# Kernel tuning notes

Hardware: AMD Instinct MI355X
Metric: run time of the kernel (lower is better)

Reference implementation:

```python
import jax, jax.numpy as jnp
import numpy as np

N = 100000      # nodes
E = 600000      # directed edges (reciprocal pairs)
D_NODE = 128    # node feature dim (== hidden, required by torch.where broadcast)
D_BOND = 16     # bond feature dim
HID = 128       # hidden size
DEPTH = 3       # message passing depth


def setup_inputs() -> dict:
    key = jax.random.key(0)
    ks = jax.random.split(key, 8)
    x = jax.random.normal(ks[0], (N, D_NODE), jnp.float32)
    # build edges as reciprocal pairs: edge 2i = (u,v), edge 2i+1 = (v,u)
    half = E // 2
    u = jax.random.randint(ks[1], (half,), 0, N)
    v = jax.random.randint(ks[2], (half,), 0, N)
    src = jnp.stack([u, v], axis=1).reshape(-1)
    dst = jnp.stack([v, u], axis=1).reshape(-1)
    edge_index = jnp.stack([src, dst])          # [2, E]
    rev_edge_index = jnp.arange(E) ^ 1           # reverse edge of 2i is 2i+1
    edge_attr = jax.random.normal(ks[3], (E, D_BOND), jnp.float32)
    # learned params (Linear: y = x @ W + b)
    s_i = 1.0 / np.sqrt(D_NODE + D_BOND)
    s_h = 1.0 / np.sqrt(HID)
    s_o = 1.0 / np.sqrt(D_NODE + HID)
    W_i = jax.random.normal(ks[4], (D_NODE + D_BOND, HID), jnp.float32) * s_i
    b_i = jnp.zeros((HID,), jnp.float32)
    W_h = jax.random.normal(ks[5], (HID, HID), jnp.float32) * s_h
    b_h = jnp.zeros((HID,), jnp.float32)
    W_o = jax.random.normal(ks[6], (D_NODE + HID, HID), jnp.float32) * s_o
    b_o = jnp.zeros((HID,), jnp.float32)
    return dict(x=x, edge_attr=edge_attr, W_i=W_i, b_i=b_i, W_h=W_h, b_h=b_h,
                W_o=W_o, b_o=b_o, edge_index=edge_index,
                rev_edge_index=rev_edge_index)


def reference(x, edge_attr, W_i, b_i, W_h, b_h, W_o, b_o,
              edge_index, rev_edge_index):
    src, dst = edge_index[0], edge_index[1]
    # H_0 = relu(W_i([x[src]; edge_attr]))
    H0 = jax.nn.relu(jnp.concatenate([x[src], edge_attr], axis=1) @ W_i + b_i)
    H = H0
    for _ in range(DEPTH - 1):
        # message: scatter-sum over dst, gather by src, subtract reverse edge
        agg = jax.ops.segment_sum(H, dst, num_segments=N)   # [N, HID]
        M = agg[src] - H[rev_edge_index]                    # [E, HID]
        # update: relu(H0 + W_h(M))   (dropout is identity in eval)
        H = jax.nn.relu(H0 + M @ W_h + b_h)
    # final node aggregation
    Mn = jax.ops.segment_sum(H, dst, num_segments=N)        # [N, HID]
    Mn = jnp.where(jnp.sum(Mn, axis=1, keepdims=True) == 0, x, Mn)
    out = jax.nn.relu(jnp.concatenate([x, Mn], axis=1) @ W_o + b_o)  # [N, HID]
    return out
```

## Files before the change

kernel.cpp:

```cpp
#include <hip/hip_runtime.h>
#include <hip/hip_bf16.h>

#define N_NODES 100000
#define N_EDGES 600000
#define HID 128
#define D_BOND 16
#define NB_CHUNKS 98

typedef __attribute__((ext_vector_type(8))) short bf16x8;
typedef __attribute__((ext_vector_type(4))) float f32x4;

__device__ __forceinline__ float bf2f(unsigned int u) {
    return __uint_as_float((u & 0xffffu) << 16);
}
__device__ __forceinline__ unsigned short f2bf(float f) {
    unsigned int x = __float_as_uint(f);
    x += 0x7fffu + ((x >> 16) & 1u);
    return (unsigned short)(x >> 16);
}
__device__ __forceinline__ unsigned int pk2(float a, float b) {
    return (unsigned int)f2bf(a) | ((unsigned int)f2bf(b) << 16);
}

__device__ __forceinline__ void st16(unsigned char* tile, int row, int u, uint4 v) {
    *reinterpret_cast<uint4*>(tile + ((row * 512 + u * 16) ^ ((row & 7) << 4))) = v;
}
__device__ __forceinline__ bf16x8 ld_a(const unsigned char* tile, int row, int kbyte) {
    return *reinterpret_cast<const bf16x8*>(tile + ((row * 512 + kbyte) ^ ((row & 7) << 4)));
}

template<int NK>
__device__ __forceinline__ void gemm_frag(const unsigned char* tile, const unsigned short* Wp,
                                          int wr, int cb, int l, f32x4 (&acc)[4]) {
    const int arow = 16 * wr + (l & 15);
    const int abyte0 = (l >> 4) * 16;
#pragma unroll
    for (int kk = 0; kk < NK; ++kk) {
        const bf16x8 a = ld_a(tile, arow, kk * 64 + abyte0);
#pragma unroll
        for (int c = 0; c < 4; ++c) {
            const bf16x8 b = *reinterpret_cast<const bf16x8*>(&Wp[(((kk * 8) + cb + c) * 64 + l) * 8]);
            acc[c] = __builtin_amdgcn_mfma_f32_16x16x32_bf16(a, b, acc[c], 0, 0, 0);
        }
    }
}

__global__ __launch_bounds__(256) void k_hist(const int* __restrict__ dst,
                                              int* __restrict__ cnt) {
    int e = blockIdx.x * 256 + threadIdx.x;
    if (e < N_EDGES) atomicAdd(&cnt[dst[e]], 1);
}

__global__ __launch_bounds__(256) void k_blocksum(const int* __restrict__ cnt,
                                                  int* __restrict__ bsum) {
    __shared__ int red[256];
    const int b = blockIdx.x, t = threadIdx.x;
    const int base = b * 1024 + t * 4;
    int s = 0;
#pragma unroll
    for (int i = 0; i < 4; ++i) { int n = base + i; if (n < N_NODES) s += cnt[n]; }
    red[t] = s; __syncthreads();
    for (int o = 128; o > 0; o >>= 1) { if (t < o) red[t] += red[t + o]; __syncthreads(); }
    if (t == 0) bsum[b] = red[0];
}

__global__ __launch_bounds__(128) void k_scan_bsum(const int* __restrict__ bsum,
                                                   int* __restrict__ boff,
                                                   int* __restrict__ rowptr) {
    __shared__ int s[128];
    const int t = threadIdx.x;
    const int v = (t < NB_CHUNKS) ? bsum[t] : 0;
    s[t] = v; __syncthreads();
    for (int o = 1; o < 128; o <<= 1) {
        int add = 0; if (t >= o) add = s[t - o];
        __syncthreads();
        s[t] += add; __syncthreads();
    }
    if (t < NB_CHUNKS) boff[t] = s[t] - v;
    if (t == 0) rowptr[N_NODES] = N_EDGES;
}

__global__ __launch_bounds__(256) void k_scan_chunk(const int* __restrict__ cnt,
                                                    const int* __restrict__ boff,
                                                    int* __restrict__ rowptr,
                                                    int* __restrict__ wpos) {
    __shared__ int s[256];
    const int b = blockIdx.x, t = threadIdx.x;
    const int base = b * 1024 + t * 4;
    int v[4]; int ts = 0;
#pragma unroll
    for (int i = 0; i < 4; ++i) { int n = base + i; v[i] = (n < N_NODES) ? cnt[n] : 0; ts += v[i]; }
    s[t] = ts; __syncthreads();
    for (int o = 1; o < 256; o <<= 1) {
        int add = 0; if (t >= o) add = s[t - o];
        __syncthreads();
        s[t] += add; __syncthreads();
    }
    int run = s[t] - ts + boff[b];
#pragma unroll
    for (int i = 0; i < 4; ++i) {
        int n = base + i;
        if (n < N_NODES) { rowptr[n] = run; wpos[n] = run; }
        run += v[i];
    }
}

__global__ __launch_bounds__(256) void k_fill(const int* __restrict__ dst,
                                              int* __restrict__ wpos,
                                              int* __restrict__ eidx) {
    int e = blockIdx.x * 256 + threadIdx.x;
    if (e < N_EDGES) { int p = atomicAdd(&wpos[dst[e]], 1); eidx[p] = e; }
}

__global__ __launch_bounds__(256) void k_pack(const float* __restrict__ Wi,
                                              const float* __restrict__ Wh,
                                              const float* __restrict__ Wo,
                                              unsigned short* __restrict__ Pi,
                                              unsigned short* __restrict__ Ph,
                                              unsigned short* __restrict__ Po) {
    const int tid = blockIdx.x * 256 + threadIdx.x;
    const float* W; unsigned short* P; int Krows, base;
    if (tid < 2560)      { W = Wi; P = Pi; Krows = 144; base = tid; }
    else if (tid < 4608) { W = Wh; P = Ph; Krows = 128; base = tid - 2560; }
    else                 { W = Wo; P = Po; Krows = 256; base = tid - 4608; }
    const int l = base & 63, fc = base >> 6;
    const int c = fc & 7, kk = fc >> 3;
    const int col = c * 16 + (l & 15);
    const int k0 = kk * 32 + (l >> 4) * 8;
    float v[8];
#pragma unroll
    for (int j = 0; j < 8; ++j) {
        const int k = k0 + j;
        v[j] = (k < Krows) ? W[(size_t)k * HID + col] : 0.f;
    }
    uint4 o;
    o.x = pk2(v[0], v[1]); o.y = pk2(v[2], v[3]);
    o.z = pk2(v[4], v[5]); o.w = pk2(v[6], v[7]);
    *reinterpret_cast<uint4*>(&P[(size_t)base * 8]) = o;
}

__device__ __forceinline__ void stage_xe(unsigned char* tile, const float* __restrict__ x,
                                         const float* __restrict__ ea, const int* s_src,
                                         int e0, int t) {
    for (int f = t; f < 512; f += 256) {
        const int e = f >> 4, u = f & 15;
        const float* xp = &x[(size_t)s_src[e] * HID + u * 8];
        const float4 v0 = *reinterpret_cast<const float4*>(xp);
        const float4 v1 = *reinterpret_cast<const float4*>(xp + 4);
        uint4 o;
        o.x = pk2(v0.x, v0.y); o.y = pk2(v0.z, v0.w);
        o.z = pk2(v1.x, v1.y); o.w = pk2(v1.z, v1.w);
        st16(tile, e, u, o);
    }
    if (t < 64) {
        const int e = t >> 1, u = t & 1;
        const float* ep = &ea[(size_t)(e0 + e) * D_BOND + u * 8];
        const float4 v0 = *reinterpret_cast<const float4*>(ep);
        const float4 v1 = *reinterpret_cast<const float4*>(ep + 4);
        uint4 o;
        o.x = pk2(v0.x, v0.y); o.y = pk2(v0.z, v0.w);
        o.z = pk2(v1.x, v1.y); o.w = pk2(v1.z, v1.w);
        st16(tile, e, 16 + u, o);
    } else if (t < 128) {
        const int i = t - 64, e = i >> 1, u = i & 1;
        st16(tile, e, 18 + u, make_uint4(0, 0, 0, 0));
    }
}

__global__ __launch_bounds__(256) void k_h0(const float* __restrict__ x,
                                            const float* __restrict__ ea,
                                            const unsigned short* __restrict__ Pi,
                                            const float* __restrict__ bi,
                                            const int* __restrict__ src,
                                            unsigned short* __restrict__ H) {
    __shared__ __align__(16) unsigned char tile[32 * 512];
    __shared__ int s_src[32];
    const int e0 = blockIdx.x * 32;
    const int t = threadIdx.x;
    if (t < 32) s_src[t] = src[e0 + t];
    __syncthreads();
    stage_xe(tile, x, ea, s_src, e0, t);
    __syncthreads();
    const int w = t >> 6, l = t & 63;
    const int wr = w & 1, cb = (w >> 1) * 4;
    f32x4 acc[4] = {{0.f,0.f,0.f,0.f},{0.f,0.f,0.f,0.f},{0.f,0.f,0.f,0.f},{0.f,0.f,0.f,0.f}};
    gemm_frag<5>(tile, Pi, wr, cb, l, acc);
    const int frow = 16 * wr + 4 * (l >> 4);
#pragma unroll
    for (int c = 0; c < 4; ++c) {
        const int col = ((cb + c) << 4) | (l & 15);
        const float bias = bi[col];
#pragma unroll
        for (int r = 0; r < 4; ++r) {
            H[(size_t)(e0 + frow + r) * HID + col] = f2bf(fmaxf(acc[c][r] + bias, 0.f));
        }
    }
}

__global__ __launch_bounds__(256) void k_agg(const unsigned short* __restrict__ H,
                                             const int* __restrict__ rowptr,
                                             const int* __restrict__ eidx,
                                             void* __restrict__ aggv) {
    const int wid = (blockIdx.x * 256 + threadIdx.x) >> 6;
    const int lane = threadIdx.x & 63;
    if (wid >= N_NODES) return;
    const int beg = rowptr[wid], end = rowptr[wid + 1];
    float a0 = 0.f, a1 = 0.f;
    for (int j = beg; j < end; ++j) {
        const int e = eidx[j];
        const unsigned int p = *reinterpret_cast<const unsigned int*>(&H[(size_t)e * HID + lane * 2]);
        a0 += bf2f(p);
        a1 += bf2f(p >> 16);
    }
    *reinterpret_cast<unsigned int*>((char*)aggv + (size_t)wid * 512 + lane * 4) = pk2(a0, a1);
}

template<int RECOMP>
__global__ __launch_bounds__(256) void k_msg(const float* __restrict__ x,
                                             const float* __restrict__ ea,
                                             const void* __restrict__ aggv,
                                             const unsigned short* __restrict__ Pi,
                                             const float* __restrict__ bi,
                                             const unsigned short* __restrict__ Ph,
                                             const float* __restrict__ bh,
                                             const int* __restrict__ src,
                                             const int* __restrict__ rev,
                                             unsigned short* H) {
    __shared__ __align__(16) unsigned char tile[32 * 512];
    __shared__ int s_src[32], s_rev[32];
    const int e0 = blockIdx.x * 32;
    const int t = threadIdx.x;
    if (t < 32) { s_src[t] = src[e0 + t]; s_rev[t] = rev[e0 + t]; }
    __syncthreads();
    const int w = t >> 6, l = t & 63;
    const int wr = w & 1, cb = (w >> 1) * 4;
    float h0r[4][4];

    if (RECOMP) {
        stage_xe(tile, x, ea, s_src, e0, t);
        __syncthreads();
        f32x4 acc[4] = {{0.f,0.f,0.f,0.f},{0.f,0.f,0.f,0.f},{0.f,0.f,0.f,0.f},{0.f,0.f,0.f,0.f}};
        gemm_frag<5>(tile, Pi, wr, cb, l, acc);
#pragma unroll
        for (int c = 0; c < 4; ++c) {
            const float bias = bi[((cb + c) << 4) | (l & 15)];
#pragma unroll
            for (int r = 0; r < 4; ++r) h0r[c][r] = fmaxf(acc[c][r] + bias, 0.f);
        }
        __syncthreads();
    }

    for (int f = t; f < 512; f += 256) {
        const int e = f >> 4, u = f & 15;
        const unsigned short* ap =
            reinterpret_cast<const unsigned short*>((const char*)aggv + (size_t)s_src[e] * 512) + u * 8;
        const uint4 av = *reinterpret_cast<const uint4*>(ap);
        const uint4 hv = *reinterpret_cast<const uint4*>(&H[(size_t)s_rev[e] * HID + u * 8]);
        uint4 o;
        o.x = pk2(bf2f(av.x) - bf2f(hv.x), bf2f(av.x >> 16) - bf2f(hv.x >> 16));
        o.y = pk2(bf2f(av.y) - bf2f(hv.y), bf2f(av.y >> 16) - bf2f(hv.y >> 16));
        o.z = pk2(bf2f(av.z) - bf2f(hv.z), bf2f(av.z >> 16) - bf2f(hv.z >> 16));
        o.w = pk2(bf2f(av.w) - bf2f(hv.w), bf2f(av.w >> 16) - bf2f(hv.w >> 16));
        st16(tile, e, u, o);
    }
    __syncthreads();
    f32x4 acc[4] = {{0.f,0.f,0.f,0.f},{0.f,0.f,0.f,0.f},{0.f,0.f,0.f,0.f},{0.f,0.f,0.f,0.f}};
    gemm_frag<4>(tile, Ph, wr, cb, l, acc);
    const int frow = 16 * wr + 4 * (l >> 4);
#pragma unroll
    for (int c = 0; c < 4; ++c) {
        const int col = ((cb + c) << 4) | (l & 15);
        const float bias = bh[col];
#pragma unroll
        for (int r = 0; r < 4; ++r) {
            const size_t idx = (size_t)(e0 + frow + r) * HID + col;
            const float h0v = RECOMP ? h0r[c][r] : bf2f((unsigned int)H[idx]);
            H[idx] = f2bf(fmaxf(h0v + acc[c][r] + bias, 0.f));
        }
    }
}

__global__ __launch_bounds__(256) void k_out(const float* __restrict__ x,
                                             const void* aggv,
                                             const int* __restrict__ cnt,
                                             const unsigned short* __restrict__ Po,
                                             const float* __restrict__ bo,
                                             float* out) {
    __shared__ __align__(16) unsigned char tile[32 * 512];
    __shared__ int s_cnt[32];
    const int n0 = blockIdx.x * 32;
    const int t = threadIdx.x;
    if (t < 32) s_cnt[t] = cnt[n0 + t];
    __syncthreads();
    for (int f = t; f < 1024; f += 256) {
        const int e = f >> 5, u = f & 31;
        uint4 o;
        if (u >= 16 && s_cnt[e] > 0) {
            o = *reinterpret_cast<const uint4*>((const char*)aggv + (size_t)(n0 + e) * 512 + (u - 16) * 16);
        } else {
            const int k8 = (u & 15) * 8;
            const float* xp = &x[(size_t)(n0 + e) * HID + k8];
            const float4 v0 = *reinterpret_cast<const float4*>(xp);
            const float4 v1 = *reinterpret_cast<const float4*>(xp + 4);
            o.x = pk2(v0.x, v0.y); o.y = pk2(v0.z, v0.w);
            o.z = pk2(v1.x, v1.y); o.w = pk2(v1.z, v1.w);
        }
        st16(tile, e, u, o);
    }
    __syncthreads();
    const int w = t >> 6, l = t & 63;
    const int wr = w & 1, cb = (w >> 1) * 4;
    f32x4 acc[4] = {{0.f,0.f,0.f,0.f},{0.f,0.f,0.f,0.f},{0.f,0.f,0.f,0.f},{0.f,0.f,0.f,0.f}};
    gemm_frag<8>(tile, Po, wr, cb, l, acc);
    const int frow = 16 * wr + 4 * (l >> 4);
#pragma unroll
    for (int c = 0; c < 4; ++c) {
        const int col = ((cb + c) << 4) | (l & 15);
        const float bias = bo[col];
#pragma unroll
        for (int r = 0; r < 4; ++r) {
            out[(size_t)(n0 + frow + r) * HID + col] = fmaxf(acc[c][r] + bias, 0.f);
        }
    }
}

extern "C" void kernel_launch(void* const* d_in, const int* in_sizes, int n_in,
                              void* d_out, int out_size, void* d_ws, size_t ws_size,
                              hipStream_t stream) {
    const float* x  = (const float*)d_in[0];
    const float* ea = (const float*)d_in[1];
    const float* Wi = (const float*)d_in[2];
    const float* bi = (const float*)d_in[3];
    const float* Wh = (const float*)d_in[4];
    const float* bh = (const float*)d_in[5];
    const float* Wo = (const float*)d_in[6];
    const float* bo = (const float*)d_in[7];
    const int* ei   = (const int*)d_in[8];
    const int* rev  = (const int*)d_in[9];
    const int* src  = ei;
    const int* dst  = ei + N_EDGES;

    char* ws = (char*)d_ws;
    size_t off = 0;
    auto alloc = [&](size_t bytes) -> void* {
        void* p = ws + off;
        off += (bytes + 255) & ~(size_t)255;
        return p;
    };
    unsigned short* H  = (unsigned short*)alloc((size_t)N_EDGES * HID * 2);
    int* cnt     = (int*)alloc((size_t)N_NODES * 4);
    int* rowptr  = (int*)alloc((size_t)(N_NODES + 1) * 4);
    int* wpos    = (int*)alloc((size_t)N_NODES * 4);
    int* bsum    = (int*)alloc(512);
    int* boff    = (int*)alloc(512);
    int* eidx    = (int*)alloc((size_t)N_EDGES * 4);
    unsigned short* Pi = (unsigned short*)alloc(2560 * 8 * 2);
    unsigned short* Ph = (unsigned short*)alloc(2048 * 8 * 2);
    unsigned short* Po = (unsigned short*)alloc(4096 * 8 * 2);
    void* agg = d_out;

    const int EB = (N_EDGES + 255) / 256;

    hipMemsetAsync(cnt, 0, (size_t)N_NODES * 4, stream);
    k_hist<<<EB, 256, 0, stream>>>(dst, cnt);
    k_blocksum<<<NB_CHUNKS, 256, 0, stream>>>(cnt, bsum);
    k_scan_bsum<<<1, 128, 0, stream>>>(bsum, boff, rowptr);
    k_scan_chunk<<<NB_CHUNKS, 256, 0, stream>>>(cnt, boff, rowptr, wpos);
    k_fill<<<EB, 256, 0, stream>>>(dst, wpos, eidx);

    k_pack<<<34, 256, 0, stream>>>(Wi, Wh, Wo, Pi, Ph, Po);

    k_h0<<<N_EDGES / 32, 256, 0, stream>>>(x, ea, Pi, bi, src, H);

    k_agg<<<N_NODES / 4, 256, 0, stream>>>(H, rowptr, eidx, agg);
    k_msg<0><<<N_EDGES / 32, 256, 0, stream>>>(x, ea, agg, Pi, bi, Ph, bh, src, rev, H);

    k_agg<<<N_NODES / 4, 256, 0, stream>>>(H, rowptr, eidx, agg);
    k_msg<1><<<N_EDGES / 32, 256, 0, stream>>>(x, ea, agg, Pi, bi, Ph, bh, src, rev, H);

    k_agg<<<N_NODES / 4, 256, 0, stream>>>(H, rowptr, eidx, agg);
    k_out<<<N_NODES / 32, 256, 0, stream>>>(x, agg, cnt, Po, bo, (float*)d_out);
}
```

Measured before the change: 674.2 us.

## Pre-convert x to bf16 and process 64-edge tiles per block

```diff
diff --git a/kernel.cpp b/kernel.cpp
--- a/kernel.cpp
+++ b/kernel.cpp
@@ -41,6 +41,24 @@
         for (int c = 0; c < 4; ++c) {
             const bf16x8 b = *reinterpret_cast<const bf16x8*>(&Wp[(((kk * 8) + cb + c) * 64 + l) * 8]);
             acc[c] = __builtin_amdgcn_mfma_f32_16x16x32_bf16(a, b, acc[c], 0, 0, 0);
+        }
+    }
+}
+
+template<int NK>
+__device__ __forceinline__ void gemm_frag2(const unsigned char* tile, const unsigned short* Wp,
+                                           int wr0, int cb, int l, f32x4 (&acc)[2][4]) {
+    const int abyte0 = (l >> 4) * 16;
+    const int ar0 = 16 * wr0 + (l & 15);
+#pragma unroll
+    for (int kk = 0; kk < NK; ++kk) {
+        const bf16x8 a0 = ld_a(tile, ar0, kk * 64 + abyte0);
+        const bf16x8 a1 = ld_a(tile, ar0 + 16, kk * 64 + abyte0);
+#pragma unroll
+        for (int c = 0; c < 4; ++c) {
+            const bf16x8 b = *reinterpret_cast<const bf16x8*>(&Wp[(((kk * 8) + cb + c) * 64 + l) * 8]);
+            acc[0][c] = __builtin_amdgcn_mfma_f32_16x16x32_bf16(a0, b, acc[0][c], 0, 0, 0);
+            acc[1][c] = __builtin_amdgcn_mfma_f32_16x16x32_bf16(a1, b, acc[1][c], 0, 0, 0);
         }
     }
 }
@@ -110,6 +128,17 @@
                                               int* __restrict__ eidx) {
     int e = blockIdx.x * 256 + threadIdx.x;
     if (e < N_EDGES) { int p = atomicAdd(&wpos[dst[e]], 1); eidx[p] = e; }
+}
+
+__global__ __launch_bounds__(256) void k_xcvt(const float* __restrict__ x,
+                                              unsigned short* __restrict__ xbf) {
+    const size_t i = (size_t)(blockIdx.x * 256 + threadIdx.x) * 8;
+    const float4 v0 = *reinterpret_cast<const float4*>(&x[i]);
+    const float4 v1 = *reinterpret_cast<const float4*>(&x[i + 4]);
+    uint4 o;
+    o.x = pk2(v0.x, v0.y); o.y = pk2(v0.z, v0.w);
+    o.z = pk2(v1.x, v1.y); o.w = pk2(v1.z, v1.w);
+    *reinterpret_cast<uint4*>(&xbf[i]) = o;
 }
 
 __global__ __launch_bounds__(256) void k_pack(const float* __restrict__ Wi,
@@ -139,20 +168,16 @@
     *reinterpret_cast<uint4*>(&P[(size_t)base * 8]) = o;
 }
 
-__device__ __forceinline__ void stage_xe(unsigned char* tile, const float* __restrict__ x,
-                                         const float* __restrict__ ea, const int* s_src,
-                                         int e0, int t) {
-    for (int f = t; f < 512; f += 256) {
+__device__ __forceinline__ void stage_xe64(unsigned char* tile, const unsigned short* __restrict__ xbf,
+                                           const float* __restrict__ ea, const int* s_src,
+                                           int e0, int t) {
+#pragma unroll
+    for (int f = t; f < 1024; f += 256) {
         const int e = f >> 4, u = f & 15;
-        const float* xp = &x[(size_t)s_src[e] * HID + u * 8];
-        const float4 v0 = *reinterpret_cast<const float4*>(xp);
-        const float4 v1 = *reinterpret_cast<const float4*>(xp + 4);
-        uint4 o;
-        o.x = pk2(v0.x, v0.y); o.y = pk2(v0.z, v0.w);
-        o.z = pk2(v1.x, v1.y); o.w = pk2(v1.z, v1.w);
-        st16(tile, e, u, o);
-    }
-    if (t < 64) {
+        const uint4 v = *reinterpret_cast<const uint4*>(&xbf[(size_t)s_src[e] * HID + u * 8]);
+        st16(tile, e, u, v);
+    }
+    if (t < 128) {
         const int e = t >> 1, u = t & 1;
         const float* ep = &ea[(size_t)(e0 + e) * D_BOND + u * 8];
         const float4 v0 = *reinterpret_cast<const float4*>(ep);
@@ -161,38 +186,41 @@
         o.x = pk2(v0.x, v0.y); o.y = pk2(v0.z, v0.w);
         o.z = pk2(v1.x, v1.y); o.w = pk2(v1.z, v1.w);
         st16(tile, e, 16 + u, o);
-    } else if (t < 128) {
-        const int i = t - 64, e = i >> 1, u = i & 1;
+    } else {
+        const int i = t - 128, e = i >> 1, u = i & 1;
         st16(tile, e, 18 + u, make_uint4(0, 0, 0, 0));
     }
 }
 
-__global__ __launch_bounds__(256) void k_h0(const float* __restrict__ x,
+__global__ __launch_bounds__(256) void k_h0(const unsigned short* __restrict__ xbf,
                                             const float* __restrict__ ea,
                                             const unsigned short* __restrict__ Pi,
                                             const float* __restrict__ bi,
                                             const int* __restrict__ src,
                                             unsigned short* __restrict__ H) {
-    __shared__ __align__(16) unsigned char tile[32 * 512];
-    __shared__ int s_src[32];
-    const int e0 = blockIdx.x * 32;
+    __shared__ __align__(16) unsigned char tile[64 * 512];
+    __shared__ int s_src[64];
+    const int e0 = blockIdx.x * 64;
     const int t = threadIdx.x;
-    if (t < 32) s_src[t] = src[e0 + t];
-    __syncthreads();
-    stage_xe(tile, x, ea, s_src, e0, t);
+    if (t < 64) s_src[t] = src[e0 + t];
+    __syncthreads();
+    stage_xe64(tile, xbf, ea, s_src, e0, t);
     __syncthreads();
     const int w = t >> 6, l = t & 63;
-    const int wr = w & 1, cb = (w >> 1) * 4;
-    f32x4 acc[4] = {{0.f,0.f,0.f,0.f},{0.f,0.f,0.f,0.f},{0.f,0.f,0.f,0.f},{0.f,0.f,0.f,0.f}};
-    gemm_frag<5>(tile, Pi, wr, cb, l, acc);
-    const int frow = 16 * wr + 4 * (l >> 4);
-#pragma unroll
-    for (int c = 0; c < 4; ++c) {
-        const int col = ((cb + c) << 4) | (l & 15);
-        const float bias = bi[col];
-#pragma unroll
-        for (int r = 0; r < 4; ++r) {
-            H[(size_t)(e0 + frow + r) * HID + col] = f2bf(fmaxf(acc[c][r] + bias, 0.f));
+    const int cb = (w & 1) * 4, wr0 = (w >> 1) * 2;
+    f32x4 acc[2][4] = {};
+    gemm_frag2<5>(tile, Pi, wr0, cb, l, acc);
+#pragma unroll
+    for (int r = 0; r < 2; ++r) {
+        const int frow = 16 * (wr0 + r) + 4 * (l >> 4);
+#pragma unroll
+        for (int c = 0; c < 4; ++c) {
+            const int col = ((cb + c) << 4) | (l & 15);
+            const float bias = bi[col];
+#pragma unroll
+            for (int rr = 0; rr < 4; ++rr) {
+                H[(size_t)(e0 + frow + rr) * HID + col] = f2bf(fmaxf(acc[r][c][rr] + bias, 0.f));
+            }
         }
     }
 }
@@ -216,7 +244,7 @@
 }
 
 template<int RECOMP>
-__global__ __launch_bounds__(256) void k_msg(const float* __restrict__ x,
+__global__ __launch_bounds__(256) void k_msg(const unsigned short* __restrict__ xbf,
                                              const float* __restrict__ ea,
                                              const void* __restrict__ aggv,
                                              const unsigned short* __restrict__ Pi,
@@ -226,31 +254,34 @@
                                              const int* __restrict__ src,
                                              const int* __restrict__ rev,
                                              unsigned short* H) {
-    __shared__ __align__(16) unsigned char tile[32 * 512];
-    __shared__ int s_src[32], s_rev[32];
-    const int e0 = blockIdx.x * 32;
+    __shared__ __align__(16) unsigned char tile[64 * 512];
+    __shared__ int s_src[64], s_rev[64];
+    const int e0 = blockIdx.x * 64;
     const int t = threadIdx.x;
-    if (t < 32) { s_src[t] = src[e0 + t]; s_rev[t] = rev[e0 + t]; }
+    if (t < 64) { s_src[t] = src[e0 + t]; s_rev[t] = rev[e0 + t]; }
     __syncthreads();
     const int w = t >> 6, l = t & 63;
-    const int wr = w & 1, cb = (w >> 1) * 4;
-    float h0r[4][4];
+    const int cb = (w & 1) * 4, wr0 = (w >> 1) * 2;
+    float h0r[2][4][4];
 
     if (RECOMP) {
-        stage_xe(tile, x, ea, s_src, e0, t);
+        stage_xe64(tile, xbf, ea, s_src, e0, t);
         __syncthreads();
-        f32x4 acc[4] = {{0.f,0.f,0.f,0.f},{0.f,0.f,0.f,0.f},{0.f,0.f,0.f,0.f},{0.f,0.f,0.f,0.f}};
-        gemm_frag<5>(tile, Pi, wr, cb, l, acc);
-#pragma unroll
-        for (int c = 0; c < 4; ++c) {
-            const float bias = bi[((cb + c) << 4) | (l & 15)];
-#pragma unroll
-            for (int r = 0; r < 4; ++r) h0r[c][r] = fmaxf(acc[c][r] + bias, 0.f);
-        }
+        f32x4 acc[2][4] = {};
+        gemm_frag2<5>(tile, Pi, wr0, cb, l, acc);
+#pragma unroll
+        for (int r = 0; r < 2; ++r)
+#pragma unroll
+            for (int c = 0; c < 4; ++c) {
+                const float bias = bi[((cb + c) << 4) | (l & 15)];
+#pragma unroll
+                for (int rr = 0; rr < 4; ++rr) h0r[r][c][rr] = fmaxf(acc[r][c][rr] + bias, 0.f);
+            }
         __syncthreads();
     }
 
-    for (int f = t; f < 512; f += 256) {
+#pragma unroll
+    for (int f = t; f < 1024; f += 256) {
         const int e = f >> 4, u = f & 15;
         const unsigned short* ap =
             reinterpret_cast<const unsigned short*>((const char*)aggv + (size_t)s_src[e] * 512) + u * 8;
@@ -264,18 +295,21 @@
         st16(tile, e, u, o);
     }
     __syncthreads();
-    f32x4 acc[4] = {{0.f,0.f,0.f,0.f},{0.f,0.f,0.f,0.f},{0.f,0.f,0.f,0.f},{0.f,0.f,0.f,0.f}};
-    gemm_frag<4>(tile, Ph, wr, cb, l, acc);
-    const int frow = 16 * wr + 4 * (l >> 4);
-#pragma unroll
-    for (int c = 0; c < 4; ++c) {
-        const int col = ((cb + c) << 4) | (l & 15);
-        const float bias = bh[col];
-#pragma unroll
-        for (int r = 0; r < 4; ++r) {
-            const size_t idx = (size_t)(e0 + frow + r) * HID + col;
-            const float h0v = RECOMP ? h0r[c][r] : bf2f((unsigned int)H[idx]);
-            H[idx] = f2bf(fmaxf(h0v + acc[c][r] + bias, 0.f));
+    f32x4 acc[2][4] = {};
+    gemm_frag2<4>(tile, Ph, wr0, cb, l, acc);
+#pragma unroll
+    for (int r = 0; r < 2; ++r) {
+        const int frow = 16 * (wr0 + r) + 4 * (l >> 4);
+#pragma unroll
+        for (int c = 0; c < 4; ++c) {
+            const int col = ((cb + c) << 4) | (l & 15);
+            const float bias = bh[col];
+#pragma unroll
+            for (int rr = 0; rr < 4; ++rr) {
+                const size_t idx = (size_t)(e0 + frow + rr) * HID + col;
+                const float h0v = RECOMP ? h0r[r][c][rr] : bf2f((unsigned int)H[idx]);
+                H[idx] = f2bf(fmaxf(h0v + acc[r][c][rr] + bias, 0.f));
+            }
         }
     }
 }
@@ -310,7 +344,7 @@
     __syncthreads();
     const int w = t >> 6, l = t & 63;
     const int wr = w & 1, cb = (w >> 1) * 4;
-    f32x4 acc[4] = {{0.f,0.f,0.f,0.f},{0.f,0.f,0.f,0.f},{0.f,0.f,0.f,0.f},{0.f,0.f,0.f,0.f}};
+    f32x4 acc[4] = {};
     gemm_frag<8>(tile, Po, wr, cb, l, acc);
     const int frow = 16 * wr + 4 * (l >> 4);
 #pragma unroll
@@ -348,6 +382,7 @@
         return p;
     };
     unsigned short* H  = (unsigned short*)alloc((size_t)N_EDGES * HID * 2);
+    unsigned short* xbf = (unsigned short*)alloc((size_t)N_NODES * HID * 2);
     int* cnt     = (int*)alloc((size_t)N_NODES * 4);
     int* rowptr  = (int*)alloc((size_t)(N_NODES + 1) * 4);
     int* wpos    = (int*)alloc((size_t)N_NODES * 4);
@@ -368,15 +403,16 @@
     k_scan_chunk<<<NB_CHUNKS, 256, 0, stream>>>(cnt, boff, rowptr, wpos);
     k_fill<<<EB, 256, 0, stream>>>(dst, wpos, eidx);
 
+    k_xcvt<<<6250, 256, 0, stream>>>(x, xbf);
     k_pack<<<34, 256, 0, stream>>>(Wi, Wh, Wo, Pi, Ph, Po);
 
-    k_h0<<<N_EDGES / 32, 256, 0, stream>>>(x, ea, Pi, bi, src, H);
+    k_h0<<<N_EDGES / 64, 256, 0, stream>>>(xbf, ea, Pi, bi, src, H);
 
     k_agg<<<N_NODES / 4, 256, 0, stream>>>(H, rowptr, eidx, agg);
-    k_msg<0><<<N_EDGES / 32, 256, 0, stream>>>(x, ea, agg, Pi, bi, Ph, bh, src, rev, H);
+    k_msg<0><<<N_EDGES / 64, 256, 0, stream>>>(xbf, ea, agg, Pi, bi, Ph, bh, src, rev, H);
 
     k_agg<<<N_NODES / 4, 256, 0, stream>>>(H, rowptr, eidx, agg);
-    k_msg<1><<<N_EDGES / 32, 256, 0, stream>>>(x, ea, agg, Pi, bi, Ph, bh, src, rev, H);
+    k_msg<1><<<N_EDGES / 64, 256, 0, stream>>>(xbf, ea, agg, Pi, bi, Ph, bh, src, rev, H);
 
     k_agg<<<N_NODES / 4, 256, 0, stream>>>(H, rowptr, eidx, agg);
     k_out<<<N_NODES / 32, 256, 0, stream>>>(x, agg, cnt, Po, bo, (float*)d_out);
```

Result: no change. 672.8 us (-0.2%).
